# Optimization experiments

Measured on AMD Instinct MI355X. Metric: run time of the kernel, lower is better.

## Reference

```python
import jax, jax.numpy as jnp
import numpy as np

B, S, D = 4, 512, 2048      # batch, seq, hidden
DFF = 5632                   # SwiGLU intermediate
E, TOPK, R = 8, 2, 16        # experts, top-k, lora rank
SCALE = 32.0 / 16.0          # lora alpha / r


def setup_inputs() -> dict:
    key = jax.random.key(0)
    ks = jax.random.split(key, 18)
    rn = lambda k, shape, s=0.02: (jax.random.normal(k, shape, dtype=jnp.float32) * s)
    return {
        "data": jax.random.normal(ks[0], (B, S, D), dtype=jnp.float32),
        # shared base SwiGLU MLP (gate/up/down projections)
        "W1": rn(ks[1], (DFF, D)),
        "W3": rn(ks[2], (DFF, D)),
        "W2": rn(ks[3], (D, DFF)),
        # MixLoRA MoE adapter: router gate + per-expert LoRA on w1/w3/w2
        "gate_W": rn(ks[4], (E, D)),
        "A1": rn(ks[5], (E, R, D)), "B1": rn(ks[6], (E, DFF, R)),
        "A3": rn(ks[7], (E, R, D)), "B3": rn(ks[8], (E, DFF, R)),
        "A2": rn(ks[9], (E, R, DFF)), "B2": rn(ks[10], (E, D, R)),
        # plain LoRA adapter (second batch segment, _lora_forward path)
        "la1": rn(ks[11], (R, D)), "lb1": rn(ks[12], (DFF, R)),
        "la3": rn(ks[13], (R, D)), "lb3": rn(ks[14], (DFF, R)),
        "la2": rn(ks[15], (R, DFF)), "lb2": rn(ks[16], (D, R)),
    }


def reference(data, W1, W3, W2, gate_W, A1, B1, A3, B3, A2, B2,
              la1, lb1, la3, lb3, la2, lb2):
    half = B // 2

    # ---- segment 0: MixLoRA MoE adapter ----
    x = data[:half].reshape(-1, D)                      # [N, D] tokens
    N = x.shape[0]
    logits = x @ gate_W.T                               # [N, E] router logits
    probs = jax.nn.softmax(logits, axis=-1)
    topw, topi = jax.lax.top_k(probs, TOPK)
    topw = topw / jnp.sum(topw, axis=-1, keepdims=True)
    # dense routing weights (zero for non-selected experts)
    wd = jnp.zeros((N, E), x.dtype).at[jnp.arange(N)[:, None], topi].set(topw)

    bg = x @ W1.T                                       # [N, DFF] base gate proj
    bu = x @ W3.T                                       # [N, DFF] base up proj
    dg = jnp.einsum('enr,efr->enf', jnp.einsum('nd,erd->enr', x, A1), B1)
    du = jnp.einsum('enr,efr->enf', jnp.einsum('nd,erd->enr', x, A3), B3)
    h = jax.nn.silu(bg[None] + SCALE * dg) * (bu[None] + SCALE * du)  # [E,N,DFF]
    oe = jnp.einsum('enf,df->end', h, W2) \
        + SCALE * jnp.einsum('enr,edr->end', jnp.einsum('enf,erf->enr', h, A2), B2)
    moe_out = jnp.einsum('ne,end->nd', wd, oe).reshape(half, S, D)

    # ---- segment 1: plain LoRA adapter (_lora_forward) ----
    x2 = data[half:]                                    # [half, S, D]
    g2 = jax.nn.silu(x2 @ W1.T + SCALE * ((x2 @ la1.T) @ lb1.T))
    u2 = x2 @ W3.T + SCALE * ((x2 @ la3.T) @ lb3.T)
    h2 = g2 * u2
    out2 = h2 @ W2.T + SCALE * ((h2 @ la2.T) @ lb2.T)

    # index_copy over contiguous per-segment ranges == concat along dim 0
    final = jnp.concatenate([moe_out, out2], axis=0)    # [B, S, D]
    return final, logits
```

## Files before the change

### kernel.cpp

```cpp
#include <hip/hip_runtime.h>
#include <hip/hip_bf16.h>

#define DEVI __device__ __forceinline__

typedef __attribute__((ext_vector_type(8))) short short8;
typedef __attribute__((ext_vector_type(4))) float f32x4;

constexpr int D    = 2048;
constexpr int DFF  = 5632;
constexpr int NTOK = 2048;
constexpr int NMOE = 1024;
constexpr float KSCALE = 2.0f;

constexpr int NW      = 11648;
constexpr int COL_A1  = 11264;
constexpr int COL_A3  = 11392;
constexpr int COL_LA1 = 11520;
constexpr int COL_LA3 = 11536;

DEVI float bf2f(unsigned short u) { return __uint_as_float(((unsigned)u) << 16); }
DEVI unsigned short f2bf(float f) {
  unsigned u = __float_as_uint(f);
  u += 0x7FFFu + ((u >> 16) & 1u);
  return (unsigned short)(u >> 16);
}
DEVI float silu(float x) { return x / (1.f + __expf(-x)); }

struct CastSegs {
  const float* src[14];
  unsigned short* dst[14];
  int blk_end[14];
};

__global__ __launch_bounds__(256) void cast_segs_kernel(CastSegs cs) {
  int b = blockIdx.x;
  int s = 0;
  #pragma unroll
  for (int i = 0; i < 14; ++i) if (b >= cs.blk_end[i]) s = i + 1;
  int bstart = (s == 0) ? 0 : cs.blk_end[s - 1];
  size_t idx = ((size_t)(b - bstart) * 256 + threadIdx.x) * 4;
  float4 v = *(const float4*)(cs.src[s] + idx);
  ushort4 o;
  o.x = f2bf(v.x); o.y = f2bf(v.y); o.z = f2bf(v.z); o.w = f2bf(v.w);
  *(ushort4*)(cs.dst[s] + idx) = o;
}

__global__ __launch_bounds__(256) void transpose_ra_kernel(const float* __restrict__ A2,
                                                           const float* __restrict__ la2,
                                                           unsigned short* __restrict__ A2tb,
                                                           unsigned short* __restrict__ la2tb) {
  int f = blockIdx.x * 256 + threadIdx.x;
  int e = blockIdx.y;
  const float* src = (e < 8) ? (A2 + (size_t)e * 16 * DFF) : la2;
  unsigned short* dst = (e < 8) ? (A2tb + (size_t)e * DFF * 16) : la2tb;
  unsigned short tmp[16];
  #pragma unroll
  for (int r = 0; r < 16; ++r) tmp[r] = f2bf(src[(size_t)r * DFF + f]);
  #pragma unroll
  for (int r = 0; r < 16; ++r) dst[(size_t)f * 16 + r] = tmp[r];
}

__global__ __launch_bounds__(256) void gate_kernel(const float* __restrict__ x,
                                                   const float* __restrict__ gW,
                                                   float* __restrict__ logits_out,
                                                   int* __restrict__ gidx,
                                                   float* __restrict__ gwt) {
  int t = blockIdx.x * 4 + (threadIdx.x >> 6);
  int lane = threadIdx.x & 63;
  const float* xr = x + (size_t)t * D;
  float acc[8];
  #pragma unroll
  for (int e = 0; e < 8; ++e) acc[e] = 0.f;
  for (int k = lane; k < D; k += 64) {
    float xv = xr[k];
    #pragma unroll
    for (int e = 0; e < 8; ++e) acc[e] = fmaf(xv, gW[e * D + k], acc[e]);
  }
  #pragma unroll
  for (int e = 0; e < 8; ++e) {
    float v = acc[e];
    #pragma unroll
    for (int s = 32; s > 0; s >>= 1) v += __shfl_xor(v, s);
    acc[e] = v;
  }
  if (lane == 0) {
    #pragma unroll
    for (int e = 0; e < 8; ++e) logits_out[(size_t)t * 8 + e] = acc[e];
    int i1 = 0;
    #pragma unroll
    for (int e = 1; e < 8; ++e) if (acc[e] > acc[i1]) i1 = e;
    int i2 = (i1 == 0) ? 1 : 0;
    #pragma unroll
    for (int e = 0; e < 8; ++e) if (e != i1 && acc[e] > acc[i2]) i2 = e;
    float w1 = 1.f / (1.f + expf(acc[i2] - acc[i1]));
    gidx[t * 2] = i1; gidx[t * 2 + 1] = i2;
    gwt[t * 2] = w1;  gwt[t * 2 + 1] = 1.f - w1;
  }
}

typedef const void __attribute__((address_space(1)))* gp1_t;
typedef void __attribute__((address_space(3)))* lp3_t;
DEVI void gload_lds16(const void* g, void* l) {
  __builtin_amdgcn_global_load_lds((gp1_t)g, (lp3_t)l, 16, 0, 0);
}
#define S_BARRIER() asm volatile("s_barrier" ::: "memory")

template <int N> DEVI void vmcnt_() {
  static_assert(N == 0 || N == 8, "enumerate literals");
  if constexpr (N == 0) asm volatile("s_waitcnt vmcnt(0)" ::: "memory");
  if constexpr (N == 8) asm volatile("s_waitcnt vmcnt(8)" ::: "memory");
}

template <int BM, int BN, int WM, int WN, int MINW, int EPI>
__global__ __launch_bounds__(WM * WN * 64, MINW) void gemmM(
    const unsigned short* __restrict__ A,
    const unsigned short* __restrict__ B,
    int K,
    float* __restrict__ Cf,
    unsigned short* __restrict__ Cb,
    const float* __restrict__ addv,
    int ldc, int nby) {
  constexpr int THREADS = WM * WN * 64;
  constexpr int RW = BM / WM;
  constexpr int CW = BN / WN;
  static_assert(RW == 64 && CW == 64, "template assumes 64x64 per-wave tile");
  constexpr int ATILE = BM * 128;
  constexpr int BTILE = BN * 128;
  constexpr int SLOT = ATILE + BTILE;
  constexpr int APARTS = BM * 8 / THREADS;
  constexpr int BPARTS = BN * 8 / THREADS;
  static_assert(APARTS + BPARTS == 8, "vmcnt gate literal assumes 8 loads/tile");

  __shared__ __align__(16) char smem[2 * SLOT];

  const int tid = threadIdx.x;
  const int wave = tid >> 6, lane = tid & 63;
  const int wm = wave / WN, wn = wave % WN;
  const int r15 = lane & 15, g = lane >> 4;

  const int nwg = (int)gridDim.x;
  const int bid = (int)blockIdx.x;
  const int wgid = (bid & 7) * (nwg >> 3) + (bid >> 3);
  const int by = wgid % nby, bx = wgid / nby;

  const unsigned short* Ablk = A + (size_t)by * BM * K;
  const unsigned short* Bblk = B + (size_t)bx * BN * K;

  int sgoA[APARTS], sgoB[BPARTS];
  #pragma unroll
  for (int j = 0; j < APARTS; ++j) {
    int tt = j * THREADS + tid;
    int row = tt >> 3;
    sgoA[j] = row * K + (((tt & 7) ^ (row & 7)) << 3);
  }
  #pragma unroll
  for (int j = 0; j < BPARTS; ++j) {
    int tt = j * THREADS + tid;
    int row = tt >> 3;
    sgoB[j] = row * K + (((tt & 7) ^ (row & 7)) << 3);
  }
  auto stage = [&](int p, int k0) {
    char* s = smem + p * SLOT;
    #pragma unroll
    for (int j = 0; j < APARTS; ++j)
      gload_lds16((const char*)Ablk + ((size_t)(sgoA[j] + k0) << 1),
                  s + j * (THREADS * 16) + wave * 1024);
    #pragma unroll
    for (int j = 0; j < BPARTS; ++j)
      gload_lds16((const char*)Bblk + ((size_t)(sgoB[j] + k0) << 1),
                  s + ATILE + j * (THREADS * 16) + wave * 1024);
  };

  const int arow0 = (wm * RW + r15) * 128;
  const int brow0 = (wn * CW + r15) * 128;
  const int s0 = ((g ^ (r15 & 7)) << 4);
  const int s1 = (((4 + g) ^ (r15 & 7)) << 4);

  f32x4 acc[4][4];
  #pragma unroll
  for (int m = 0; m < 4; ++m)
    #pragma unroll
    for (int n = 0; n < 4; ++n)
      #pragma unroll
      for (int j = 0; j < 4; ++j) acc[m][n][j] = 0.f;

  const int NT = K >> 6;

  stage(0, 0);

  for (int t = 0; t < NT; ++t) {
    const int p = t & 1;
    if (t + 1 < NT) {
      stage(p ^ 1, (t + 1) << 6);
      vmcnt_<8>();
    } else {
      vmcnt_<0>();
    }
    S_BARRIER();

    const char* sA = smem + p * SLOT;
    const char* sB = sA + ATILE;

    short8 bq[4][2], av[4][2];
    #pragma unroll
    for (int n = 0; n < 4; ++n) {
      bq[n][0] = *(const short8*)(sB + brow0 + n * 2048 + s0);
      bq[n][1] = *(const short8*)(sB + brow0 + n * 2048 + s1);
    }
    #pragma unroll
    for (int m = 0; m < 4; ++m) {
      av[m][0] = *(const short8*)(sA + arow0 + m * 2048 + s0);
      av[m][1] = *(const short8*)(sA + arow0 + m * 2048 + s1);
    }
    #pragma unroll
    for (int m = 0; m < 4; ++m)
      #pragma unroll
      for (int n = 0; n < 4; ++n)
        #pragma unroll
        for (int kk = 0; kk < 2; ++kk)
          acc[m][n] = __builtin_amdgcn_mfma_f32_16x16x32_bf16(
              av[m][kk], bq[n][kk], acc[m][n], 0, 0, 0);

    S_BARRIER();
  }

  const int row0 = by * BM + wm * RW + (g << 2);
  const int col0 = bx * BN + wn * CW + r15;
  #pragma unroll
  for (int m = 0; m < 4; ++m) {
    #pragma unroll
    for (int n = 0; n < 4; ++n) {
      int col = col0 + n * 16;
      #pragma unroll
      for (int j = 0; j < 4; ++j) {
        int row = row0 + m * 16 + j;
        size_t off = (size_t)row * ldc + col;
        float v = acc[m][n][j];
        if (EPI == 1) Cb[off] = f2bf(v);
        else          Cf[off] = v + addv[off];
      }
    }
  }
}

DEVI float dot16bf(const float* a, const unsigned short* w) {
  short8 w0 = *(const short8*)w;
  short8 w1 = *(const short8*)(w + 8);
  float s = 0.f;
  #pragma unroll
  for (int i = 0; i < 8; ++i) s = fmaf(a[i],     bf2f((unsigned short)w0[i]), s);
  #pragma unroll
  for (int i = 0; i < 8; ++i) s = fmaf(a[8 + i], bf2f((unsigned short)w1[i]), s);
  return s;
}

__global__ __launch_bounds__(256) void h_kernel(
    const unsigned short* __restrict__ GU,
    const unsigned short* __restrict__ B1b,
    const unsigned short* __restrict__ B3b,
    const unsigned short* __restrict__ A2tb,
    const unsigned short* __restrict__ lb1b,
    const unsigned short* __restrict__ lb3b,
    const unsigned short* __restrict__ la2tb,
    const int* __restrict__ gidx, const float* __restrict__ gwt,
    unsigned short* __restrict__ Hb,
    float* __restrict__ qw) {
  const int t = blockIdx.x;
  const int tid = threadIdx.x;
  const unsigned short* gu = GU + (size_t)t * NW;
  unsigned short* hrow = Hb + (size_t)t * DFF;
  float qacc[32];
  #pragma unroll
  for (int r = 0; r < 32; ++r) qacc[r] = 0.f;
  float w1 = 0.f, w2 = 0.f;

  if (t < NMOE) {
    const int e1 = gidx[t * 2], e2 = gidx[t * 2 + 1];
    w1 = gwt[t * 2]; w2 = gwt[t * 2 + 1];
    float xa1a[16], xa1b[16], xa3a[16], xa3b[16];
    #pragma unroll
    for (int r = 0; r < 16; ++r) {
      xa1a[r] = bf2f(gu[COL_A1 + e1 * 16 + r]);
      xa1b[r] = bf2f(gu[COL_A1 + e2 * 16 + r]);
      xa3a[r] = bf2f(gu[COL_A3 + e1 * 16 + r]);
      xa3b[r] = bf2f(gu[COL_A3 + e2 * 16 + r]);
    }
    const unsigned short* B1e1 = B1b + (size_t)e1 * DFF * 16;
    const unsigned short* B1e2 = B1b + (size_t)e2 * DFF * 16;
    const unsigned short* B3e1 = B3b + (size_t)e1 * DFF * 16;
    const unsigned short* B3e2 = B3b + (size_t)e2 * DFF * 16;
    const unsigned short* A2e1 = A2tb + (size_t)e1 * DFF * 16;
    const unsigned short* A2e2 = A2tb + (size_t)e2 * DFF * 16;
    for (int i = 0; i < 22; ++i) {
      int f = tid + i * 256;
      float bg = bf2f(gu[f]), bu = bf2f(gu[DFF + f]);
      float dg1 = dot16bf(xa1a, B1e1 + f * 16);
      float du1 = dot16bf(xa3a, B3e1 + f * 16);
      float dg2 = dot16bf(xa1b, B1e2 + f * 16);
      float du2 = dot16bf(xa3b, B3e2 + f * 16);
      float h1 = silu(bg + KSCALE * dg1) * (bu + KSCALE * du1);
      float h2 = silu(bg + KSCALE * dg2) * (bu + KSCALE * du2);
      hrow[f] = f2bf(w1 * h1 + w2 * h2);
      short8 a0 = *(const short8*)(A2e1 + f * 16);
      short8 a1 = *(const short8*)(A2e1 + f * 16 + 8);
      short8 b0 = *(const short8*)(A2e2 + f * 16);
      short8 b1 = *(const short8*)(A2e2 + f * 16 + 8);
      #pragma unroll
      for (int r = 0; r < 8; ++r) {
        qacc[r]      = fmaf(h1, bf2f((unsigned short)a0[r]), qacc[r]);
        qacc[8 + r]  = fmaf(h1, bf2f((unsigned short)a1[r]), qacc[8 + r]);
        qacc[16 + r] = fmaf(h2, bf2f((unsigned short)b0[r]), qacc[16 + r]);
        qacc[24 + r] = fmaf(h2, bf2f((unsigned short)b1[r]), qacc[24 + r]);
      }
    }
  } else {
    float s1[16], s3[16];
    #pragma unroll
    for (int r = 0; r < 16; ++r) {
      s1[r] = bf2f(gu[COL_LA1 + r]);
      s3[r] = bf2f(gu[COL_LA3 + r]);
    }
    for (int i = 0; i < 22; ++i) {
      int f = tid + i * 256;
      float bg = bf2f(gu[f]), bu = bf2f(gu[DFF + f]);
      float dg = dot16bf(s1, lb1b + f * 16);
      float du = dot16bf(s3, lb3b + f * 16);
      float h = silu(bg + KSCALE * dg) * (bu + KSCALE * du);
      hrow[f] = f2bf(h);
      short8 a0 = *(const short8*)(la2tb + f * 16);
      short8 a1 = *(const short8*)(la2tb + f * 16 + 8);
      #pragma unroll
      for (int r = 0; r < 8; ++r) {
        qacc[r]     = fmaf(h, bf2f((unsigned short)a0[r]), qacc[r]);
        qacc[8 + r] = fmaf(h, bf2f((unsigned short)a1[r]), qacc[8 + r]);
      }
    }
  }

  #pragma unroll
  for (int r = 0; r < 32; ++r) {
    float v = qacc[r];
    #pragma unroll
    for (int s = 32; s > 0; s >>= 1) v += __shfl_xor(v, s);
    qacc[r] = v;
  }
  __shared__ float red[4][32];
  const int wave = tid >> 6, lane = tid & 63;
  if (lane == 0) {
    #pragma unroll
    for (int r = 0; r < 32; ++r) red[wave][r] = qacc[r];
  }
  __syncthreads();
  if (tid < 32) {
    float v = red[0][tid] + red[1][tid] + red[2][tid] + red[3][tid];
    float sc = (t < NMOE) ? ((tid < 16) ? (KSCALE * w1) : (KSCALE * w2)) : KSCALE;
    qw[(size_t)t * 32 + tid] = v * sc;
  }
}

__global__ __launch_bounds__(256) void ylora_kernel(const float* __restrict__ qw,
                                                    const unsigned short* __restrict__ B2b,
                                                    const unsigned short* __restrict__ lb2b,
                                                    const int* __restrict__ gidx,
                                                    float* __restrict__ ylora) {
  const int t = blockIdx.x;
  const int tid = threadIdx.x;
  const float* qr = qw + (size_t)t * 32;
  float q1[16], q2[16];
  #pragma unroll
  for (int r = 0; r < 16; ++r) { q1[r] = qr[r]; q2[r] = qr[16 + r]; }
  if (t < NMOE) {
    const unsigned short* p1 = B2b + (size_t)gidx[t * 2] * D * 16;
    const unsigned short* p2 = B2b + (size_t)gidx[t * 2 + 1] * D * 16;
    #pragma unroll
    for (int i = 0; i < 8; ++i) {
      int d = tid + i * 256;
      ylora[(size_t)t * D + d] = dot16bf(q1, p1 + d * 16) + dot16bf(q2, p2 + d * 16);
    }
  } else {
    #pragma unroll
    for (int i = 0; i < 8; ++i) {
      int d = tid + i * 256;
      ylora[(size_t)t * D + d] = dot16bf(q1, lb2b + d * 16);
    }
  }
}

extern "C" void kernel_launch(void* const* d_in, const int* in_sizes, int n_in,
                              void* d_out, int out_size, void* d_ws, size_t ws_size,
                              hipStream_t stream) {
  (void)in_sizes; (void)n_in; (void)out_size; (void)ws_size;
  const float* data = (const float*)d_in[0];
  const float* W1   = (const float*)d_in[1];
  const float* W3   = (const float*)d_in[2];
  const float* W2   = (const float*)d_in[3];
  const float* gW   = (const float*)d_in[4];
  const float* A1   = (const float*)d_in[5];
  const float* B1   = (const float*)d_in[6];
  const float* A3   = (const float*)d_in[7];
  const float* B3   = (const float*)d_in[8];
  const float* A2   = (const float*)d_in[9];
  const float* B2   = (const float*)d_in[10];
  const float* la1  = (const float*)d_in[11];
  const float* lb1  = (const float*)d_in[12];
  const float* la3  = (const float*)d_in[13];
  const float* lb3  = (const float*)d_in[14];
  const float* la2  = (const float*)d_in[15];
  const float* lb2  = (const float*)d_in[16];

  char* w = (char*)d_ws;
  size_t off = 0;
  auto alloc = [&](size_t bytes) -> char* {
    char* p = w + off;
    off += (bytes + 255) & ~(size_t)255;
    return p;
  };
  unsigned short* xb    = (unsigned short*)alloc((size_t)NTOK * D * 2);
  unsigned short* W13b  = (unsigned short*)alloc((size_t)NW * D * 2);
  unsigned short* W2b   = (unsigned short*)alloc((size_t)D * DFF * 2);
  unsigned short* B1b   = (unsigned short*)alloc((size_t)8 * DFF * 16 * 2);
  unsigned short* B3b   = (unsigned short*)alloc((size_t)8 * DFF * 16 * 2);
  unsigned short* A2tb  = (unsigned short*)alloc((size_t)8 * DFF * 16 * 2);
  unsigned short* la2tb = (unsigned short*)alloc((size_t)DFF * 16 * 2);
  unsigned short* lb1b  = (unsigned short*)alloc((size_t)DFF * 16 * 2);
  unsigned short* lb3b  = (unsigned short*)alloc((size_t)DFF * 16 * 2);
  unsigned short* lb2b  = (unsigned short*)alloc((size_t)D * 16 * 2);
  unsigned short* B2b   = (unsigned short*)alloc((size_t)8 * D * 16 * 2);
  int*   gidx = (int*)alloc((size_t)NMOE * 2 * 4);
  float* gwt  = (float*)alloc((size_t)NMOE * 2 * 4);
  unsigned short* GU    = (unsigned short*)alloc((size_t)NTOK * NW * 2);

  unsigned short* Hb = W13b;
  float* ylora = (float*)((char*)W13b + (size_t)NTOK * DFF * 2);
  float* qw    = (float*)xb;

  CastSegs cs;
  const float* srcs[14] = {data, W1, W3, W2, A1, A3, la1, la3, B1, B3, lb1, lb3, lb2, B2};
  unsigned short* dsts[14] = {
      xb, W13b, W13b + (size_t)DFF * D, W2b,
      W13b + (size_t)COL_A1 * D, W13b + (size_t)COL_A3 * D,
      W13b + (size_t)COL_LA1 * D, W13b + (size_t)COL_LA3 * D,
      B1b, B3b, lb1b, lb3b, lb2b, B2b};
  int ns[14] = {NTOK * D, DFF * D, DFF * D, DFF * D, 128 * D, 128 * D, 16 * D, 16 * D,
                8 * DFF * 16, 8 * DFF * 16, DFF * 16, DFF * 16, D * 16, 8 * D * 16};
  int total_blocks = 0;
  for (int i = 0; i < 14; ++i) {
    cs.src[i] = srcs[i];
    cs.dst[i] = dsts[i];
    total_blocks += ns[i] / 1024;
    cs.blk_end[i] = total_blocks;
  }
  cast_segs_kernel<<<total_blocks, 256, 0, stream>>>(cs);
  transpose_ra_kernel<<<dim3(DFF / 256, 9), 256, 0, stream>>>(A2, la2, A2tb, la2tb);
  hipMemsetAsync(W13b + (size_t)11552 * D, 0, (size_t)(NW - 11552) * D * 2, stream);

  gate_kernel<<<NMOE / 4, 256, 0, stream>>>(data, gW,
      (float*)d_out + (size_t)NTOK * D, gidx, gwt);

  gemmM<128, 128, 2, 2, 2, 1><<<(NTOK / 128) * (NW / 128), 256, 0, stream>>>(
      xb, W13b, D, (float*)nullptr, GU, (const float*)nullptr, NW, NTOK / 128);

  h_kernel<<<NTOK, 256, 0, stream>>>(GU, B1b, B3b, A2tb, lb1b, lb3b, la2tb,
                                     gidx, gwt, Hb, qw);

  ylora_kernel<<<NTOK, 256, 0, stream>>>(qw, B2b, lb2b, gidx, ylora);

  gemmM<128, 128, 2, 2, 2, 2><<<(NTOK / 128) * (D / 128), 256, 0, stream>>>(
      Hb, W2b, DFF, (float*)d_out, (unsigned short*)nullptr, ylora, D, NTOK / 128);
}
```

Baseline: 341.2 us.

## Fold LoRA down-projections into augmented-K GEMMs and drop ylora pass

Pads the K dimension of both GEMMs (2048→2112, 5632→5824) and writes the LoRA B factors (lb1/lb3, per-expert B2, lb2) into the extra weight columns. The scaled LoRA intermediates (x·la, routed h·A2) are written into the matching activation columns, so the tensor-core GEMMs compute the LoRA contributions directly. This removes the ylora kernel, the fp32 ylora buffer round trip, the dot-product work in h_kernel's LoRA branch, and the add in the GEMM epilogue. In exchange it adds extra K work in both GEMMs, several new cast kernels, and a small xla reduction kernel. The LoRA intermediates are also now rounded to bf16 before use. EPI 3 is used, and it maps to the plain-store branch.

Result: slower. 461.9 us (+35.4%).

```diff
diff --git a/kernel.cpp b/kernel.cpp
--- a/kernel.cpp
+++ b/kernel.cpp
@@ -12,11 +12,11 @@
 constexpr int NMOE = 1024;
 constexpr float KSCALE = 2.0f;
 
-constexpr int NW      = 11648;
-constexpr int COL_A1  = 11264;
-constexpr int COL_A3  = 11392;
-constexpr int COL_LA1 = 11520;
-constexpr int COL_LA3 = 11536;
+constexpr int KA = 2112;
+constexpr int KH = 5824;
+constexpr int NW     = 11648;
+constexpr int COL_A1 = 11264;
+constexpr int COL_A3 = 11392;
 
 DEVI float bf2f(unsigned short u) { return __uint_as_float(((unsigned)u) << 16); }
 DEVI unsigned short f2bf(float f) {
@@ -26,23 +26,151 @@
 }
 DEVI float silu(float x) { return x / (1.f + __expf(-x)); }
 
-struct CastSegs {
-  const float* src[14];
-  unsigned short* dst[14];
-  int blk_end[14];
-};
-
-__global__ __launch_bounds__(256) void cast_segs_kernel(CastSegs cs) {
+__global__ __launch_bounds__(256) void cast_x_kernel(const float* __restrict__ data,
+                                                     unsigned short* __restrict__ xb) {
+  const int row = blockIdx.x, tid = threadIdx.x;
+  const float* src = data + (size_t)row * D;
+  unsigned short* dst = xb + (size_t)row * KA;
+  const int c = tid * 8;
+  float4 v0 = *(const float4*)(src + c);
+  float4 v1 = *(const float4*)(src + c + 4);
+  ushort4 o0, o1;
+  o0.x = f2bf(v0.x); o0.y = f2bf(v0.y); o0.z = f2bf(v0.z); o0.w = f2bf(v0.w);
+  o1.x = f2bf(v1.x); o1.y = f2bf(v1.y); o1.z = f2bf(v1.z); o1.w = f2bf(v1.w);
+  *(ushort4*)(dst + c) = o0;
+  *(ushort4*)(dst + c + 4) = o1;
+  if (tid < 16) {
+    ushort4 z; z.x = 0; z.y = 0; z.z = 0; z.w = 0;
+    *(ushort4*)(dst + D + tid * 4) = z;
+  }
+}
+
+__global__ __launch_bounds__(256) void xla_kernel(const float* __restrict__ data,
+                                                  const float* __restrict__ la1,
+                                                  const float* __restrict__ la3,
+                                                  unsigned short* __restrict__ xb) {
+  const int t = blockIdx.x * 4 + (threadIdx.x >> 6);
+  const int lane = threadIdx.x & 63;
+  const float* xr = data + (size_t)(NMOE + t) * D;
+  float acc[32];
+  #pragma unroll
+  for (int r = 0; r < 32; ++r) acc[r] = 0.f;
+  for (int k = lane; k < D; k += 64) {
+    float xv = xr[k];
+    #pragma unroll
+    for (int r = 0; r < 16; ++r) {
+      acc[r]      = fmaf(xv, la1[r * D + k], acc[r]);
+      acc[16 + r] = fmaf(xv, la3[r * D + k], acc[16 + r]);
+    }
+  }
+  #pragma unroll
+  for (int r = 0; r < 32; ++r) {
+    float v = acc[r];
+    #pragma unroll
+    for (int s = 32; s > 0; s >>= 1) v += __shfl_xor(v, s);
+    acc[r] = v;
+  }
+  if (lane == 0) {
+    unsigned short* dst = xb + (size_t)(NMOE + t) * KA + D;
+    #pragma unroll
+    for (int r = 0; r < 32; ++r) dst[r] = f2bf(KSCALE * acc[r]);
+  }
+}
+
+__global__ __launch_bounds__(256) void cast_wlb_kernel(const float* __restrict__ W1,
+                                                       const float* __restrict__ W3,
+                                                       const float* __restrict__ lb1,
+                                                       const float* __restrict__ lb3,
+                                                       unsigned short* __restrict__ Wt) {
+  const int f = blockIdx.x;
+  const int tid = threadIdx.x;
+  const bool isW1 = f < DFF;
+  const float* src = isW1 ? (W1 + (size_t)f * D) : (W3 + (size_t)(f - DFF) * D);
+  unsigned short* dst = Wt + (size_t)f * KA;
+  const int c = tid * 8;
+  float4 v0 = *(const float4*)(src + c);
+  float4 v1 = *(const float4*)(src + c + 4);
+  ushort4 o0, o1;
+  o0.x = f2bf(v0.x); o0.y = f2bf(v0.y); o0.z = f2bf(v0.z); o0.w = f2bf(v0.w);
+  o1.x = f2bf(v1.x); o1.y = f2bf(v1.y); o1.z = f2bf(v1.z); o1.w = f2bf(v1.w);
+  *(ushort4*)(dst + c) = o0;
+  *(ushort4*)(dst + c + 4) = o1;
+  if (tid < 16) {
+    unsigned short o[4];
+    #pragma unroll
+    for (int j = 0; j < 4; ++j) {
+      int rel = tid * 4 + j;
+      float v = 0.f;
+      if (isW1 && rel < 16)                 v = lb1[(size_t)f * 16 + rel];
+      if (!isW1 && rel >= 16 && rel < 32)   v = lb3[(size_t)(f - DFF) * 16 + (rel - 16)];
+      o[j] = f2bf(v);
+    }
+    ushort4 ov; ov.x = o[0]; ov.y = o[1]; ov.z = o[2]; ov.w = o[3];
+    *(ushort4*)(dst + D + tid * 4) = ov;
+  }
+}
+
+__global__ __launch_bounds__(256) void cast_a13_kernel(const float* __restrict__ A1,
+                                                       const float* __restrict__ A3,
+                                                       unsigned short* __restrict__ Wt) {
+  const int b = blockIdx.x;
+  const int tid = threadIdx.x;
+  const float* src = (b < 128) ? (A1 + (size_t)b * D) : (A3 + (size_t)(b - 128) * D);
+  unsigned short* dst = Wt + (size_t)(COL_A1 + b) * KA;
+  const int c = tid * 8;
+  float4 v0 = *(const float4*)(src + c);
+  float4 v1 = *(const float4*)(src + c + 4);
+  ushort4 o0, o1;
+  o0.x = f2bf(v0.x); o0.y = f2bf(v0.y); o0.z = f2bf(v0.z); o0.w = f2bf(v0.w);
+  o1.x = f2bf(v1.x); o1.y = f2bf(v1.y); o1.z = f2bf(v1.z); o1.w = f2bf(v1.w);
+  *(ushort4*)(dst + c) = o0;
+  *(ushort4*)(dst + c + 4) = o1;
+  if (tid < 16) {
+    ushort4 z; z.x = 0; z.y = 0; z.z = 0; z.w = 0;
+    *(ushort4*)(dst + D + tid * 4) = z;
+  }
+}
+
+__global__ __launch_bounds__(256) void cast_w2_kernel(const float* __restrict__ W2,
+                                                      const float* __restrict__ B2,
+                                                      const float* __restrict__ lb2,
+                                                      unsigned short* __restrict__ W2t) {
+  const int d = blockIdx.x, tid = threadIdx.x;
+  const float* src = W2 + (size_t)d * DFF;
+  unsigned short* dst = W2t + (size_t)d * KH;
+  for (int c = tid * 4; c < DFF; c += 1024) {
+    float4 v = *(const float4*)(src + c);
+    ushort4 o;
+    o.x = f2bf(v.x); o.y = f2bf(v.y); o.z = f2bf(v.z); o.w = f2bf(v.w);
+    *(ushort4*)(dst + c) = o;
+  }
+  if (tid < 48) {
+    unsigned short o[4];
+    #pragma unroll
+    for (int j = 0; j < 4; ++j) {
+      int rel = tid * 4 + j;
+      float v = 0.f;
+      if (rel < 128)      v = B2[(size_t)(rel >> 4) * D * 16 + (size_t)d * 16 + (rel & 15)];
+      else if (rel < 144) v = lb2[(size_t)d * 16 + (rel - 128)];
+      o[j] = f2bf(v);
+    }
+    ushort4 ov; ov.x = o[0]; ov.y = o[1]; ov.z = o[2]; ov.w = o[3];
+    *(ushort4*)(dst + DFF + tid * 4) = ov;
+  }
+}
+
+__global__ __launch_bounds__(256) void cast_flat2_kernel(const float* __restrict__ B1,
+                                                         const float* __restrict__ B3,
+                                                         unsigned short* __restrict__ B1b,
+                                                         unsigned short* __restrict__ B3b) {
   int b = blockIdx.x;
-  int s = 0;
-  #pragma unroll
-  for (int i = 0; i < 14; ++i) if (b >= cs.blk_end[i]) s = i + 1;
-  int bstart = (s == 0) ? 0 : cs.blk_end[s - 1];
-  size_t idx = ((size_t)(b - bstart) * 256 + threadIdx.x) * 4;
-  float4 v = *(const float4*)(cs.src[s] + idx);
+  const float* src; unsigned short* dst;
+  if (b < 704) { src = B1; dst = B1b; } else { src = B3; dst = B3b; b -= 704; }
+  size_t idx = ((size_t)b * 256 + threadIdx.x) * 4;
+  float4 v = *(const float4*)(src + idx);
   ushort4 o;
   o.x = f2bf(v.x); o.y = f2bf(v.y); o.z = f2bf(v.z); o.w = f2bf(v.w);
-  *(ushort4*)(cs.dst[s] + idx) = o;
+  *(ushort4*)(dst + idx) = o;
 }
 
 __global__ __launch_bounds__(256) void transpose_ra_kernel(const float* __restrict__ A2,
@@ -118,7 +246,6 @@
     int K,
     float* __restrict__ Cf,
     unsigned short* __restrict__ Cb,
-    const float* __restrict__ addv,
     int ldc, int nby) {
   constexpr int THREADS = WM * WN * 64;
   constexpr int RW = BM / WM;
@@ -237,7 +364,7 @@
         size_t off = (size_t)row * ldc + col;
         float v = acc[m][n][j];
         if (EPI == 1) Cb[off] = f2bf(v);
-        else          Cf[off] = v + addv[off];
+        else          Cf[off] = v;
       }
     }
   }
@@ -246,12 +373,13 @@
 DEVI float dot16bf(const float* a, const unsigned short* w) {
   short8 w0 = *(const short8*)w;
   short8 w1 = *(const short8*)(w + 8);
-  float s = 0.f;
-  #pragma unroll
-  for (int i = 0; i < 8; ++i) s = fmaf(a[i],     bf2f((unsigned short)w0[i]), s);
-  #pragma unroll
-  for (int i = 0; i < 8; ++i) s = fmaf(a[8 + i], bf2f((unsigned short)w1[i]), s);
-  return s;
+  float s0 = 0.f, s1 = 0.f;
+  #pragma unroll
+  for (int i = 0; i < 8; ++i) {
+    s0 = fmaf(a[i],     bf2f((unsigned short)w0[i]), s0);
+    s1 = fmaf(a[8 + i], bf2f((unsigned short)w1[i]), s1);
+  }
+  return s0 + s1;
 }
 
 __global__ __launch_bounds__(256) void h_kernel(
@@ -259,23 +387,21 @@
     const unsigned short* __restrict__ B1b,
     const unsigned short* __restrict__ B3b,
     const unsigned short* __restrict__ A2tb,
-    const unsigned short* __restrict__ lb1b,
-    const unsigned short* __restrict__ lb3b,
     const unsigned short* __restrict__ la2tb,
     const int* __restrict__ gidx, const float* __restrict__ gwt,
-    unsigned short* __restrict__ Hb,
-    float* __restrict__ qw) {
+    unsigned short* __restrict__ Hb) {
   const int t = blockIdx.x;
   const int tid = threadIdx.x;
   const unsigned short* gu = GU + (size_t)t * NW;
-  unsigned short* hrow = Hb + (size_t)t * DFF;
+  unsigned short* hrow = Hb + (size_t)t * KH;
   float qacc[32];
   #pragma unroll
   for (int r = 0; r < 32; ++r) qacc[r] = 0.f;
+  int e1 = 0, e2 = 1;
   float w1 = 0.f, w2 = 0.f;
 
   if (t < NMOE) {
-    const int e1 = gidx[t * 2], e2 = gidx[t * 2 + 1];
+    e1 = gidx[t * 2]; e2 = gidx[t * 2 + 1];
     w1 = gwt[t * 2]; w2 = gwt[t * 2 + 1];
     float xa1a[16], xa1b[16], xa3a[16], xa3b[16];
     #pragma unroll
@@ -314,18 +440,10 @@
       }
     }
   } else {
-    float s1[16], s3[16];
-    #pragma unroll
-    for (int r = 0; r < 16; ++r) {
-      s1[r] = bf2f(gu[COL_LA1 + r]);
-      s3[r] = bf2f(gu[COL_LA3 + r]);
-    }
     for (int i = 0; i < 22; ++i) {
       int f = tid + i * 256;
       float bg = bf2f(gu[f]), bu = bf2f(gu[DFF + f]);
-      float dg = dot16bf(s1, lb1b + f * 16);
-      float du = dot16bf(s3, lb3b + f * 16);
-      float h = silu(bg + KSCALE * dg) * (bu + KSCALE * du);
+      float h = silu(bg) * bu;
       hrow[f] = f2bf(h);
       short8 a0 = *(const short8*)(la2tb + f * 16);
       short8 a1 = *(const short8*)(la2tb + f * 16 + 8);
@@ -351,38 +469,16 @@
     for (int r = 0; r < 32; ++r) red[wave][r] = qacc[r];
   }
   __syncthreads();
-  if (tid < 32) {
-    float v = red[0][tid] + red[1][tid] + red[2][tid] + red[3][tid];
-    float sc = (t < NMOE) ? ((tid < 16) ? (KSCALE * w1) : (KSCALE * w2)) : KSCALE;
-    qw[(size_t)t * 32 + tid] = v * sc;
-  }
-}
-
-__global__ __launch_bounds__(256) void ylora_kernel(const float* __restrict__ qw,
-                                                    const unsigned short* __restrict__ B2b,
-                                                    const unsigned short* __restrict__ lb2b,
-                                                    const int* __restrict__ gidx,
-                                                    float* __restrict__ ylora) {
-  const int t = blockIdx.x;
-  const int tid = threadIdx.x;
-  const float* qr = qw + (size_t)t * 32;
-  float q1[16], q2[16];
-  #pragma unroll
-  for (int r = 0; r < 16; ++r) { q1[r] = qr[r]; q2[r] = qr[16 + r]; }
-  if (t < NMOE) {
-    const unsigned short* p1 = B2b + (size_t)gidx[t * 2] * D * 16;
-    const unsigned short* p2 = B2b + (size_t)gidx[t * 2 + 1] * D * 16;
-    #pragma unroll
-    for (int i = 0; i < 8; ++i) {
-      int d = tid + i * 256;
-      ylora[(size_t)t * D + d] = dot16bf(q1, p1 + d * 16) + dot16bf(q2, p2 + d * 16);
-    }
-  } else {
-    #pragma unroll
-    for (int i = 0; i < 8; ++i) {
-      int d = tid + i * 256;
-      ylora[(size_t)t * D + d] = dot16bf(q1, lb2b + d * 16);
-    }
+  if (tid < 192) {
+    int e = tid >> 4, r = tid & 15;
+    float v = 0.f;
+    if (t < NMOE) {
+      if (e == e1)      v = KSCALE * w1 * (red[0][r] + red[1][r] + red[2][r] + red[3][r]);
+      else if (e == e2) v = KSCALE * w2 * (red[0][16 + r] + red[1][16 + r] + red[2][16 + r] + red[3][16 + r]);
+    } else {
+      if (e == 8)       v = KSCALE * (red[0][r] + red[1][r] + red[2][r] + red[3][r]);
+    }
+    hrow[DFF + tid] = f2bf(v);
   }
 }
 
@@ -415,56 +511,37 @@
     off += (bytes + 255) & ~(size_t)255;
     return p;
   };
-  unsigned short* xb    = (unsigned short*)alloc((size_t)NTOK * D * 2);
-  unsigned short* W13b  = (unsigned short*)alloc((size_t)NW * D * 2);
-  unsigned short* W2b   = (unsigned short*)alloc((size_t)D * DFF * 2);
+  unsigned short* xb    = (unsigned short*)alloc((size_t)NTOK * KA * 2);
+  unsigned short* W13t  = (unsigned short*)alloc((size_t)NW * KA * 2);
+  unsigned short* W2t   = (unsigned short*)alloc((size_t)D * KH * 2);
   unsigned short* B1b   = (unsigned short*)alloc((size_t)8 * DFF * 16 * 2);
   unsigned short* B3b   = (unsigned short*)alloc((size_t)8 * DFF * 16 * 2);
   unsigned short* A2tb  = (unsigned short*)alloc((size_t)8 * DFF * 16 * 2);
   unsigned short* la2tb = (unsigned short*)alloc((size_t)DFF * 16 * 2);
-  unsigned short* lb1b  = (unsigned short*)alloc((size_t)DFF * 16 * 2);
-  unsigned short* lb3b  = (unsigned short*)alloc((size_t)DFF * 16 * 2);
-  unsigned short* lb2b  = (unsigned short*)alloc((size_t)D * 16 * 2);
-  unsigned short* B2b   = (unsigned short*)alloc((size_t)8 * D * 16 * 2);
   int*   gidx = (int*)alloc((size_t)NMOE * 2 * 4);
   float* gwt  = (float*)alloc((size_t)NMOE * 2 * 4);
   unsigned short* GU    = (unsigned short*)alloc((size_t)NTOK * NW * 2);
 
-  unsigned short* Hb = W13b;
-  float* ylora = (float*)((char*)W13b + (size_t)NTOK * DFF * 2);
-  float* qw    = (float*)xb;
-
-  CastSegs cs;
-  const float* srcs[14] = {data, W1, W3, W2, A1, A3, la1, la3, B1, B3, lb1, lb3, lb2, B2};
-  unsigned short* dsts[14] = {
-      xb, W13b, W13b + (size_t)DFF * D, W2b,
-      W13b + (size_t)COL_A1 * D, W13b + (size_t)COL_A3 * D,
-      W13b + (size_t)COL_LA1 * D, W13b + (size_t)COL_LA3 * D,
-      B1b, B3b, lb1b, lb3b, lb2b, B2b};
-  int ns[14] = {NTOK * D, DFF * D, DFF * D, DFF * D, 128 * D, 128 * D, 16 * D, 16 * D,
-                8 * DFF * 16, 8 * DFF * 16, DFF * 16, DFF * 16, D * 16, 8 * D * 16};
-  int total_blocks = 0;
-  for (int i = 0; i < 14; ++i) {
-    cs.src[i] = srcs[i];
-    cs.dst[i] = dsts[i];
-    total_blocks += ns[i] / 1024;
-    cs.blk_end[i] = total_blocks;
-  }
-  cast_segs_kernel<<<total_blocks, 256, 0, stream>>>(cs);
+  unsigned short* Hb = W13t;
+
+  cast_x_kernel<<<NTOK, 256, 0, stream>>>(data, xb);
+  cast_wlb_kernel<<<2 * DFF, 256, 0, stream>>>(W1, W3, lb1, lb3, W13t);
+  cast_a13_kernel<<<256, 256, 0, stream>>>(A1, A3, W13t);
+  hipMemsetAsync(W13t + (size_t)(COL_A3 + 128) * KA, 0,
+                 (size_t)(NW - (COL_A3 + 128)) * KA * 2, stream);
+  cast_w2_kernel<<<D, 256, 0, stream>>>(W2, B2, lb2, W2t);
+  cast_flat2_kernel<<<1408, 256, 0, stream>>>(B1, B3, B1b, B3b);
   transpose_ra_kernel<<<dim3(DFF / 256, 9), 256, 0, stream>>>(A2, la2, A2tb, la2tb);
-  hipMemsetAsync(W13b + (size_t)11552 * D, 0, (size_t)(NW - 11552) * D * 2, stream);
 
   gate_kernel<<<NMOE / 4, 256, 0, stream>>>(data, gW,
       (float*)d_out + (size_t)NTOK * D, gidx, gwt);
+  xla_kernel<<<NMOE / 4, 256, 0, stream>>>(data, la1, la3, xb);
 
   gemmM<128, 128, 2, 2, 2, 1><<<(NTOK / 128) * (NW / 128), 256, 0, stream>>>(
-      xb, W13b, D, (float*)nullptr, GU, (const float*)nullptr, NW, NTOK / 128);
-
-  h_kernel<<<NTOK, 256, 0, stream>>>(GU, B1b, B3b, A2tb, lb1b, lb3b, la2tb,
-                                     gidx, gwt, Hb, qw);
-
-  ylora_kernel<<<NTOK, 256, 0, stream>>>(qw, B2b, lb2b, gidx, ylora);
-
-  gemmM<128, 128, 2, 2, 2, 2><<<(NTOK / 128) * (D / 128), 256, 0, stream>>>(
-      Hb, W2b, DFF, (float*)d_out, (unsigned short*)nullptr, ylora, D, NTOK / 128);
-}
+      xb, W13t, KA, (float*)nullptr, GU, NW, NTOK / 128);
+
+  h_kernel<<<NTOK, 256, 0, stream>>>(GU, B1b, B3b, A2tb, la2tb, gidx, gwt, Hb);
+
+  gemmM<128, 128, 2, 2, 2, 3><<<(NTOK / 128) * (D / 128), 256, 0, stream>>>(
+      Hb, W2t, KH, (float*)d_out, (unsigned short*)nullptr, D, NTOK / 128);
+}
```
